# Kernel tuning notes

Measured on AMD Instinct MI355X. Metric: run time of the kernel, lower is better.

Reference implementation:

```python
import jax, jax.numpy as jnp
from jax import lax
import numpy as np

DIM, RESO, HEADS, SPLIT, B = 128, 112, 4, 7, 2
HID = 4 * DIM  # mlp_ratio=4


def _ln(x, g, b):
    m = x.mean(-1, keepdims=True)
    v = ((x - m) ** 2).mean(-1, keepdims=True)
    return (x - m) * lax.rsqrt(v + 1e-5) * g + b


def _lepe_attn(q, k, v, cw, cb, H, W, H_sp, W_sp, nh):
    # q,k,v: [B, H*W, C] (C = branch dim); cw: depthwise conv weight [C,1,3,3]
    Bq, L, C = q.shape
    hd = C // nh
    scale = hd ** -0.5
    nHw, nWw = H // H_sp, W // W_sp

    def to_win(t):  # [B,H,W,C] -> [B*nHw*nWw, nh, H_sp*W_sp, hd]
        t = t.reshape(Bq, nHw, H_sp, nWw, W_sp, C).transpose(0, 1, 3, 2, 4, 5)
        return t.reshape(-1, H_sp * W_sp, nh, hd).transpose(0, 2, 1, 3)

    qw = to_win(q.reshape(Bq, H, W, C)) * scale
    kw = to_win(k.reshape(Bq, H, W, C))

    # v path: window partition in NCHW, depthwise conv LePE per window
    vimg = v.transpose(0, 2, 1).reshape(Bq, C, H, W)
    vimg = vimg.reshape(Bq, C, nHw, H_sp, nWw, W_sp).transpose(0, 2, 4, 1, 3, 5)
    vimg = vimg.reshape(-1, C, H_sp, W_sp)  # [B', C, H_sp, W_sp]
    lepe = lax.conv_general_dilated(vimg, cw, (1, 1), 'SAME', feature_group_count=C,
                                    dimension_numbers=('NCHW', 'OIHW', 'NCHW'))
    lepe = lepe + cb[None, :, None, None]
    vw = vimg.reshape(-1, nh, hd, H_sp * W_sp).transpose(0, 1, 3, 2)
    lepe = lepe.reshape(-1, nh, hd, H_sp * W_sp).transpose(0, 1, 3, 2)

    attn = jax.nn.softmax(jnp.einsum('whnd,whmd->whnm', qw, kw), axis=-1)
    o = jnp.einsum('whnm,whmd->whnd', attn, vw) + lepe  # [B', nh, S, hd]

    # windows2img
    o = o.transpose(0, 2, 1, 3).reshape(-1, H_sp * W_sp, C)
    o = o.reshape(Bq, nHw, nWw, H_sp, W_sp, C).transpose(0, 1, 3, 2, 4, 5)
    return o.reshape(Bq, H * W, C)


def setup_inputs() -> dict:
    key = jax.random.key(0)
    ks = jax.random.split(key, 16)
    s = 0.02
    Cb = DIM // 2
    return {
        'x': jax.random.normal(ks[0], (B, RESO * RESO, DIM), jnp.float32),
        'g1': jnp.ones((DIM,), jnp.float32),
        'b1': jnp.zeros((DIM,), jnp.float32),
        'w_qkv': s * jax.random.normal(ks[1], (3 * DIM, DIM), jnp.float32),
        'conv_w0': s * jax.random.normal(ks[2], (Cb, 1, 3, 3), jnp.float32),
        'conv_b0': jnp.zeros((Cb,), jnp.float32),
        'conv_w1': s * jax.random.normal(ks[3], (Cb, 1, 3, 3), jnp.float32),
        'conv_b1': jnp.zeros((Cb,), jnp.float32),
        'w_proj': s * jax.random.normal(ks[4], (DIM, DIM), jnp.float32),
        'b_proj': jnp.zeros((DIM,), jnp.float32),
        'g2': jnp.ones((DIM,), jnp.float32),
        'b2': jnp.zeros((DIM,), jnp.float32),
        'w_fc1': s * jax.random.normal(ks[5], (HID, DIM), jnp.float32),
        'b_fc1': jnp.zeros((HID,), jnp.float32),
        'w_fc2': s * jax.random.normal(ks[6], (DIM, HID), jnp.float32),
        'b_fc2': jnp.zeros((DIM,), jnp.float32),
    }


def reference(x, g1, b1, w_qkv, conv_w0, conv_b0, conv_w1, conv_b1,
              w_proj, b_proj, g2, b2, w_fc1, b_fc1, w_fc2, b_fc2):
    Bq, L, C = x.shape
    Cb = C // 2
    nh_b = HEADS // 2
    img = _ln(x, g1, b1)
    qkv = (img @ w_qkv.T).reshape(Bq, L, 3, C)  # qkv_bias=False
    q, k, v = qkv[:, :, 0], qkv[:, :, 1], qkv[:, :, 2]
    # branch 0: horizontal stripes (H_sp=RESO, W_sp=SPLIT) on first half of channels
    x1 = _lepe_attn(q[..., :Cb], k[..., :Cb], v[..., :Cb], conv_w0, conv_b0,
                    RESO, RESO, RESO, SPLIT, nh_b)
    # branch 1: vertical stripes (H_sp=SPLIT, W_sp=RESO) on second half
    x2 = _lepe_attn(q[..., Cb:], k[..., Cb:], v[..., Cb:], conv_w1, conv_b1,
                    RESO, RESO, SPLIT, RESO, nh_b)
    att = jnp.concatenate([x1, x2], axis=2)
    att = att @ w_proj.T + b_proj
    x = x + att  # drop_path = identity (prob 0)
    y = _ln(x, g2, b2)
    h = jax.nn.gelu(y @ w_fc1.T + b_fc1, approximate=False)
    x = x + (h @ w_fc2.T + b_fc2)
    return x
```

## Files before the change

kernel.cpp:

```cpp
#include <hip/hip_runtime.h>
#include <cstdint>

#define LTOK 12544
#define BATCH 2
#define CDIM 128
#define C3 384
#define RES 112
#define NROWS (BATCH * LTOK)
#define CHUNKS 784
#define GRID 256
#define SCALE 0.17677669529663687f

typedef __attribute__((ext_vector_type(8))) short bf16x8;
typedef __attribute__((ext_vector_type(4))) float f32x4;

__device__ inline ushort f2b(float f) {
    union { float f; unsigned u; } v; v.f = f;
    unsigned r = (v.u + 0x7FFFu + ((v.u >> 16) & 1u)) >> 16;
    return (ushort)r;
}
__device__ inline float b2f(ushort u) {
    union { float f; unsigned u; } v; v.u = ((unsigned)u) << 16; return v.f;
}
__device__ inline float gelu_f(float a) {
    float u2 = 1.5957691216f * (a + 0.044715f * a * a * a);
    return a - a / (__expf(u2) + 1.0f);
}

__device__ inline void nij(int n, int branch, int& i, int& j) {
    if (branch == 0) { i = n / 7; j = n - i * 7; }
    else             { i = n / 112; j = n - i * 112; }
}

__global__ __launch_bounds__(256) void k_cvt(const float* __restrict__ w0, const float* __restrict__ w1,
        const float* __restrict__ w2, const float* __restrict__ w3,
        ushort* __restrict__ o0, ushort* __restrict__ o1,
        ushort* __restrict__ o2, ushort* __restrict__ o3)
{
    int idx = blockIdx.x * 256 + threadIdx.x;
    const float* src; ushort* dst; int vi;
    if      (idx < 12288) { src = w0; dst = o0; vi = idx; }
    else if (idx < 16384) { src = w1; dst = o1; vi = idx - 12288; }
    else if (idx < 32768) { src = w2; dst = o2; vi = idx - 16384; }
    else                  { src = w3; dst = o3; vi = idx - 32768; }
    float4 v = ((const float4*)src)[vi];
    ushort4 r; r.x = f2b(v.x); r.y = f2b(v.y); r.z = f2b(v.z); r.w = f2b(v.w);
    ((ushort4*)dst)[vi] = r;
}

__global__ __launch_bounds__(512) void k_ln_qkv(const float* __restrict__ x,
        const float* __restrict__ g1, const float* __restrict__ b1,
        const ushort* __restrict__ wqkv_bf, ushort* __restrict__ qkv)
{
    __shared__ ushort ys[32 * 136];
    const int tid = threadIdx.x;
    const int wv = tid >> 6, lane = tid & 63;
    const int c16 = lane & 15, g = lane >> 4;

    bf16x8 wr[3][4];
    #pragma unroll
    for (int t = 0; t < 3; ++t)
        #pragma unroll
        for (int kc = 0; kc < 4; ++kc)
            wr[t][kc] = *(const bf16x8*)&wqkv_bf[(wv * 48 + t * 16 + c16) * CDIM + kc * 32 + g * 8];

    const int r = tid >> 4, l16 = tid & 15;
    float4 gv0 = *(const float4*)(g1 + l16 * 8);
    float4 gv4 = *(const float4*)(g1 + l16 * 8 + 4);
    float4 bv0 = *(const float4*)(b1 + l16 * 8);
    float4 bv4 = *(const float4*)(b1 + l16 * 8 + 4);

    for (int c = blockIdx.x; c < CHUNKS; c += GRID) {
        const long long row0 = (long long)c * 32;

        {
            const float* xr = x + (row0 + r) * CDIM + l16 * 8;
            float4 a0 = *(const float4*)xr;
            float4 a1 = *(const float4*)(xr + 4);
            float s  = a0.x + a0.y + a0.z + a0.w + a1.x + a1.y + a1.z + a1.w;
            float s2 = a0.x*a0.x + a0.y*a0.y + a0.z*a0.z + a0.w*a0.w
                     + a1.x*a1.x + a1.y*a1.y + a1.z*a1.z + a1.w*a1.w;
            #pragma unroll
            for (int m = 8; m >= 1; m >>= 1) { s += __shfl_xor(s, m, 16); s2 += __shfl_xor(s2, m, 16); }
            const float mean = s * (1.f / 128.f);
            const float var = s2 * (1.f / 128.f) - mean * mean;
            const float rs = rsqrtf(var + 1e-5f);
            ushort4 w0, w1;
            w0.x = f2b((a0.x - mean) * rs * gv0.x + bv0.x);
            w0.y = f2b((a0.y - mean) * rs * gv0.y + bv0.y);
            w0.z = f2b((a0.z - mean) * rs * gv0.z + bv0.z);
            w0.w = f2b((a0.w - mean) * rs * gv0.w + bv0.w);
            w1.x = f2b((a1.x - mean) * rs * gv4.x + bv4.x);
            w1.y = f2b((a1.y - mean) * rs * gv4.y + bv4.y);
            w1.z = f2b((a1.z - mean) * rs * gv4.z + bv4.z);
            w1.w = f2b((a1.w - mean) * rs * gv4.w + bv4.w);
            *(ushort4*)&ys[r * 136 + l16 * 8]     = w0;
            *(ushort4*)&ys[r * 136 + l16 * 8 + 4] = w1;
        }
        __syncthreads();

        bf16x8 yb[2][4];
        #pragma unroll
        for (int mt = 0; mt < 2; ++mt)
            #pragma unroll
            for (int kc = 0; kc < 4; ++kc)
                yb[mt][kc] = *(const bf16x8*)&ys[(mt * 16 + c16) * 136 + kc * 32 + g * 8];
        __syncthreads();

        #pragma unroll
        for (int t = 0; t < 3; ++t) {
            const int n0 = wv * 48 + t * 16;
            #pragma unroll
            for (int mt = 0; mt < 2; ++mt) {
                f32x4 acc = {0.f, 0.f, 0.f, 0.f};
                #pragma unroll
                for (int kc = 0; kc < 4; ++kc)
                    acc = __builtin_amdgcn_mfma_f32_16x16x32_bf16(wr[t][kc], yb[mt][kc], acc, 0, 0, 0);
                ushort4 sv;
                sv.x = f2b(acc[0]); sv.y = f2b(acc[1]); sv.z = f2b(acc[2]); sv.w = f2b(acc[3]);
                *(ushort4*)&qkv[(row0 + mt * 16 + c16) * C3 + n0 + g * 4] = sv;
            }
        }
    }
}

__global__ __launch_bounds__(448) void k_attn4(const ushort* __restrict__ qkv,
        const float* __restrict__ cw0, const float* __restrict__ cb0,
        const float* __restrict__ cw1, const float* __restrict__ cb1,
        ushort* __restrict__ att)
{
    __shared__ __align__(16) ushort ks[112 * 40];
    __shared__ __align__(16) ushort vt[32 * 136];
    __shared__ __align__(16) char pool[7][2304];

    const int tid = threadIdx.x;
    const int wv = tid >> 6, lane = tid & 63;
    const int g = lane >> 4, c16 = lane & 15;

    const int wh = blockIdx.x;
    const int branch = wh >> 6;
    const int idx = wh & 63;
    const int win = idx >> 1, head = idx & 1;
    const int b = win >> 4, w = win & 15;
    const int rowBase = branch ? w * 7 : 0;
    const int colBase = branch ? 0 : w * 7;
    const float* cw = branch ? cw1 : cw0;
    const float* cb = branch ? cb1 : cb0;
    const int cbase = branch * 64 + head * 32;
    const long long qkvB = (long long)b * LTOK * C3;

    if (tid < 256) {
        const int row = tid >> 3, cwd = tid & 7;
        *(unsigned*)&vt[row * 136 + 112 + cwd * 2] = 0u;
    }

    const int gt = blockIdx.y * 7 + wv;

    bf16x8 qq;
    {
        int n = gt * 16 + c16;
        int i, j; nij(n, branch, i, j);
        const ushort* qp = qkv + qkvB + (long long)((rowBase + i) * RES + colBase + j) * C3 + cbase + g * 8;
        qq = *(const bf16x8*)qp;
        #pragma unroll
        for (int e = 0; e < 8; ++e) qq[e] = (short)f2b(b2f((ushort)qq[e]) * SCALE);
    }

    f32x4 O0 = {0.f,0.f,0.f,0.f}, O1 = {0.f,0.f,0.f,0.f};
    float lsum[4] = {0.f,0.f,0.f,0.f};
    ushort* pb = (ushort*)pool[wv];

    for (int cc = 0; cc < 7; ++cc) {
        __syncthreads();
        {
            const int key = tid >> 2, d8 = (tid & 3) * 8;
            const int n = cc * 112 + key;
            int i, j; nij(n, branch, i, j);
            const ushort* base = qkv + qkvB + (long long)((rowBase + i) * RES + colBase + j) * C3 + cbase + d8;
            bf16x8 kk = *(const bf16x8*)(base + 128);
            bf16x8 vv = *(const bf16x8*)(base + 256);
            *(bf16x8*)&ks[key * 40 + d8] = kk;
            #pragma unroll
            for (int e = 0; e < 8; ++e) vt[(d8 + e) * 136 + key] = (ushort)vv[e];
        }
        __syncthreads();

        #pragma unroll
        for (int p = 0; p < 4; ++p) {
            bf16x8 kf0 = *(const bf16x8*)&ks[(p * 32 + c16) * 40 + g * 8];
            bf16x8 kf1;
            if (p < 3) kf1 = *(const bf16x8*)&ks[(p * 32 + 16 + c16) * 40 + g * 8];
            bf16x8 vf0 = *(const bf16x8*)&vt[c16 * 136 + p * 32 + g * 8];
            bf16x8 vf1 = *(const bf16x8*)&vt[(16 + c16) * 136 + p * 32 + g * 8];

            f32x4 z = {0.f,0.f,0.f,0.f};
            f32x4 S0 = __builtin_amdgcn_mfma_f32_16x16x32_bf16(qq, kf0, z, 0, 0, 0);
            f32x4 S1 = z;
            if (p < 3) S1 = __builtin_amdgcn_mfma_f32_16x16x32_bf16(qq, kf1, z, 0, 0, 0);
            ushort pw0[4], pw1[4];
            #pragma unroll
            for (int r = 0; r < 4; ++r) {
                float e0 = __expf(S0[r]);
                lsum[r] += e0;
                pw0[r] = f2b(e0);
                if (p < 3) {
                    float e1 = __expf(S1[r]);
                    lsum[r] += e1;
                    pw1[r] = f2b(e1);
                } else pw1[r] = 0;
            }
            #pragma unroll
            for (int r = 0; r < 4; ++r) {
                pb[(g * 4 + r) * 40 + c16]      = pw0[r];
                pb[(g * 4 + r) * 40 + 16 + c16] = pw1[r];
            }
            bf16x8 pf = *(const bf16x8*)&pb[c16 * 40 + g * 8];
            O0 = __builtin_amdgcn_mfma_f32_16x16x32_bf16(pf, vf0, O0, 0, 0, 0);
            O1 = __builtin_amdgcn_mfma_f32_16x16x32_bf16(pf, vf1, O1, 0, 0, 0);
        }
    }

    const int H_sp = branch ? 7 : RES;
    const int W_sp = branch ? RES : 7;
    float* ob = (float*)pool[wv];
    #pragma unroll
    for (int r = 0; r < 4; ++r) {
        float s = lsum[r];
        s += __shfl_xor(s, 1); s += __shfl_xor(s, 2);
        s += __shfl_xor(s, 4); s += __shfl_xor(s, 8);
        const float inv = 1.f / s;
        ob[(g * 4 + r) * 36 + c16]      = O0[r] * inv;
        ob[(g * 4 + r) * 36 + 16 + c16] = O1[r] * inv;
    }
    const int r2 = lane >> 2, db = (lane & 3) * 8;
    const int n0 = gt * 16 + r2;
    int i0, j0; nij(n0, branch, i0, j0);
    float acc[8];
    #pragma unroll
    for (int e = 0; e < 8; ++e) acc[e] = ob[r2 * 36 + db + e] + cb[head * 32 + db + e];
    #pragma unroll
    for (int dij = 0; dij < 9; ++dij) {
        const int di = dij / 3 - 1, dj = dij % 3 - 1;
        const int ii = i0 + di, jj = j0 + dj;
        if (ii >= 0 && ii < H_sp && jj >= 0 && jj < W_sp) {
            const ushort* vp = qkv + qkvB + (long long)((rowBase + ii) * RES + colBase + jj) * C3 + 256 + cbase + db;
            bf16x8 vv = *(const bf16x8*)vp;
            #pragma unroll
            for (int e = 0; e < 8; ++e)
                acc[e] += cw[(head * 32 + db + e) * 9 + dij] * b2f((ushort)vv[e]);
        }
    }
    const long long Lq = (long long)(rowBase + i0) * RES + colBase + j0;
    ushort* op = att + ((long long)b * LTOK + Lq) * CDIM + cbase + db;
    bf16x8 ov;
    #pragma unroll
    for (int e = 0; e < 8; ++e) ov[e] = (short)f2b(acc[e]);
    *(bf16x8*)op = ov;
}

__global__ __launch_bounds__(512) void k_pmlp(const ushort* __restrict__ att,
        const ushort* __restrict__ wproj_bf, const float* __restrict__ bproj,
        const float* __restrict__ x,
        const float* __restrict__ g2, const float* __restrict__ b2,
        const ushort* __restrict__ w1bf, const float* __restrict__ bfc1,
        const ushort* __restrict__ w2bf, const float* __restrict__ bfc2,
        float* __restrict__ out)
{
    __shared__ float  xs[32 * 132];
    __shared__ ushort ys[32 * 136];
    __shared__ ushort hs[32 * 520];
    const int tid = threadIdx.x;
    const int wv = tid >> 6, lane = tid & 63;
    const int c16 = lane & 15, g = lane >> 4;

    bf16x8 wpr[4];
    #pragma unroll
    for (int kc = 0; kc < 4; ++kc)
        wpr[kc] = *(const bf16x8*)&wproj_bf[(wv * 16 + c16) * CDIM + kc * 32 + g * 8];
    bf16x8 w1r[4][4];
    #pragma unroll
    for (int t = 0; t < 4; ++t)
        #pragma unroll
        for (int kc = 0; kc < 4; ++kc)
            w1r[t][kc] = *(const bf16x8*)&w1bf[(wv * 64 + t * 16 + c16) * CDIM + kc * 32 + g * 8];
    const float4 bpv = *(const float4*)&bproj[wv * 16 + g * 4];
    float4 b1v[4];
    #pragma unroll
    for (int t = 0; t < 4; ++t) b1v[t] = *(const float4*)&bfc1[wv * 64 + t * 16 + g * 4];
    const float4 b2v = *(const float4*)&bfc2[wv * 16 + g * 4];

    const int r = tid >> 4, l16 = tid & 15;
    float4 gv0 = *(const float4*)(g2 + l16 * 8);
    float4 gv4 = *(const float4*)(g2 + l16 * 8 + 4);
    float4 bv0 = *(const float4*)(b2 + l16 * 8);
    float4 bv4 = *(const float4*)(b2 + l16 * 8 + 4);

    for (int c = blockIdx.x; c < CHUNKS; c += GRID) {
        const long long row0 = (long long)c * 32;

        f32x4 resid[2];
        {
            bf16x8 ab[2][4];
            #pragma unroll
            for (int mt = 0; mt < 2; ++mt)
                #pragma unroll
                for (int kc = 0; kc < 4; ++kc)
                    ab[mt][kc] = *(const bf16x8*)&att[(row0 + mt * 16 + c16) * CDIM + kc * 32 + g * 8];
            const int col = wv * 16 + g * 4;
            #pragma unroll
            for (int mt = 0; mt < 2; ++mt) {
                f32x4 a = {0.f, 0.f, 0.f, 0.f};
                #pragma unroll
                for (int kc = 0; kc < 4; ++kc)
                    a = __builtin_amdgcn_mfma_f32_16x16x32_bf16(wpr[kc], ab[mt][kc], a, 0, 0, 0);
                float4 xv = *(const float4*)&x[(row0 + mt * 16 + c16) * CDIM + col];
                f32x4 rr;
                rr[0] = a[0] + xv.x + bpv.x;
                rr[1] = a[1] + xv.y + bpv.y;
                rr[2] = a[2] + xv.z + bpv.z;
                rr[3] = a[3] + xv.w + bpv.w;
                resid[mt] = rr;
                *(float4*)&xs[(mt * 16 + c16) * 132 + col] = make_float4(rr[0], rr[1], rr[2], rr[3]);
            }
        }
        __syncthreads();

        {
            float4 a0 = *(const float4*)&xs[r * 132 + l16 * 8];
            float4 a1 = *(const float4*)&xs[r * 132 + l16 * 8 + 4];
            float s  = a0.x + a0.y + a0.z + a0.w + a1.x + a1.y + a1.z + a1.w;
            float s2 = a0.x*a0.x + a0.y*a0.y + a0.z*a0.z + a0.w*a0.w
                     + a1.x*a1.x + a1.y*a1.y + a1.z*a1.z + a1.w*a1.w;
            #pragma unroll
            for (int m = 8; m >= 1; m >>= 1) { s += __shfl_xor(s, m, 16); s2 += __shfl_xor(s2, m, 16); }
            const float mean = s * (1.f / 128.f);
            const float var = s2 * (1.f / 128.f) - mean * mean;
            const float rs = rsqrtf(var + 1e-5f);
            ushort4 w0, w1;
            w0.x = f2b((a0.x - mean) * rs * gv0.x + bv0.x);
            w0.y = f2b((a0.y - mean) * rs * gv0.y + bv0.y);
            w0.z = f2b((a0.z - mean) * rs * gv0.z + bv0.z);
            w0.w = f2b((a0.w - mean) * rs * gv0.w + bv0.w);
            w1.x = f2b((a1.x - mean) * rs * gv4.x + bv4.x);
            w1.y = f2b((a1.y - mean) * rs * gv4.y + bv4.y);
            w1.z = f2b((a1.z - mean) * rs * gv4.z + bv4.z);
            w1.w = f2b((a1.w - mean) * rs * gv4.w + bv4.w);
            *(ushort4*)&ys[r * 136 + l16 * 8]     = w0;
            *(ushort4*)&ys[r * 136 + l16 * 8 + 4] = w1;
        }
        __syncthreads();

        bf16x8 yb[2][4];
        #pragma unroll
        for (int mt = 0; mt < 2; ++mt)
            #pragma unroll
            for (int kc = 0; kc < 4; ++kc)
                yb[mt][kc] = *(const bf16x8*)&ys[(mt * 16 + c16) * 136 + kc * 32 + g * 8];

        #pragma unroll
        for (int t = 0; t < 4; ++t) {
            #pragma unroll
            for (int mt = 0; mt < 2; ++mt) {
                f32x4 a = {0.f, 0.f, 0.f, 0.f};
                #pragma unroll
                for (int kc = 0; kc < 4; ++kc)
                    a = __builtin_amdgcn_mfma_f32_16x16x32_bf16(w1r[t][kc], yb[mt][kc], a, 0, 0, 0);
                ushort4 sv;
                sv.x = f2b(gelu_f(a[0] + b1v[t].x));
                sv.y = f2b(gelu_f(a[1] + b1v[t].y));
                sv.z = f2b(gelu_f(a[2] + b1v[t].z));
                sv.w = f2b(gelu_f(a[3] + b1v[t].w));
                *(ushort4*)&hs[(mt * 16 + c16) * 520 + wv * 64 + t * 16 + g * 4] = sv;
            }
        }

        bf16x8 w2r[16];
        #pragma unroll
        for (int kc = 0; kc < 16; ++kc)
            w2r[kc] = *(const bf16x8*)&w2bf[(wv * 16 + c16) * 512 + kc * 32 + g * 8];

        __syncthreads();

        f32x4 acc2[2] = {{0.f,0.f,0.f,0.f},{0.f,0.f,0.f,0.f}};
        #pragma unroll
        for (int kc = 0; kc < 16; ++kc) {
            bf16x8 hb[2];
            #pragma unroll
            for (int mt = 0; mt < 2; ++mt)
                hb[mt] = *(const bf16x8*)&hs[(mt * 16 + c16) * 520 + kc * 32 + g * 8];
            #pragma unroll
            for (int mt = 0; mt < 2; ++mt)
                acc2[mt] = __builtin_amdgcn_mfma_f32_16x16x32_bf16(w2r[kc], hb[mt], acc2[mt], 0, 0, 0);
        }

        {
            const int col = wv * 16 + g * 4;
            #pragma unroll
            for (int mt = 0; mt < 2; ++mt) {
                const long long row = row0 + mt * 16 + c16;
                float4 o;
                o.x = acc2[mt][0] + resid[mt][0] + b2v.x;
                o.y = acc2[mt][1] + resid[mt][1] + b2v.y;
                o.z = acc2[mt][2] + resid[mt][2] + b2v.z;
                o.w = acc2[mt][3] + resid[mt][3] + b2v.w;
                *(float4*)&out[row * CDIM + col] = o;
            }
        }
    }
}

extern "C" void kernel_launch(void* const* d_in, const int* in_sizes, int n_in,
                              void* d_out, int out_size, void* d_ws, size_t ws_size,
                              hipStream_t stream) {
    const float* x     = (const float*)d_in[0];
    const float* g1    = (const float*)d_in[1];
    const float* b1    = (const float*)d_in[2];
    const float* wqkv  = (const float*)d_in[3];
    const float* cw0   = (const float*)d_in[4];
    const float* cb0   = (const float*)d_in[5];
    const float* cw1   = (const float*)d_in[6];
    const float* cb1   = (const float*)d_in[7];
    const float* wproj = (const float*)d_in[8];
    const float* bproj = (const float*)d_in[9];
    const float* g2    = (const float*)d_in[10];
    const float* b2    = (const float*)d_in[11];
    const float* wfc1  = (const float*)d_in[12];
    const float* bfc1  = (const float*)d_in[13];
    const float* wfc2  = (const float*)d_in[14];
    const float* bfc2  = (const float*)d_in[15];

    char* wsb = (char*)d_ws;
    ushort* qkv_bf   = (ushort*)wsb;
    ushort* att_bf   = (ushort*)(wsb + 19267584);
    char*   wbase    = wsb + 19267584 + 6422528;
    ushort* wqkv_bf  = (ushort*)(wbase);
    ushort* wproj_bf = (ushort*)(wbase + 98304);
    ushort* wfc1_bf  = (ushort*)(wbase + 98304 + 32768);
    ushort* wfc2_bf  = (ushort*)(wbase + 98304 + 32768 + 131072);

    float* out = (float*)d_out;

    k_cvt<<<192, 256, 0, stream>>>(wqkv, wproj, wfc1, wfc2, wqkv_bf, wproj_bf, wfc1_bf, wfc2_bf);
    k_ln_qkv<<<GRID, 512, 0, stream>>>(x, g1, b1, wqkv_bf, qkv_bf);
    k_attn4<<<dim3(128, 7), 448, 0, stream>>>(qkv_bf, cw0, cb0, cw1, cb1, att_bf);
    k_pmlp<<<GRID, 512, 0, stream>>>(att_bf, wproj_bf, bproj, x, g2, b2,
                                     wfc1_bf, bfc1, wfc2_bf, bfc2, out);
}
```

Before: 115.7 us.

## Process two query tiles per wave, prefetch K/V, and widen MLP grids

The attention kernel now handles two 16-query tiles per wave, so each staged K/V chunk in shared memory is reused by twice as many queries, and the grid shrinks from 7 to 4 y-blocks. The next chunk's K and V are loaded into registers while the current chunk is computed, and V is transposed using paired ushort2 stores from half the threads. The QKV and MLP kernels launch 512 blocks instead of 256. The costs are more registers per thread (possible occupancy loss), idle waves in the last y-block, and fewer blocks for attention.

```diff
diff --git a/kernel.cpp b/kernel.cpp
--- a/kernel.cpp
+++ b/kernel.cpp
@@ -8,7 +8,7 @@
 #define RES 112
 #define NROWS (BATCH * LTOK)
 #define CHUNKS 784
-#define GRID 256
+#define GRID_MLP 512
 #define SCALE 0.17677669529663687f
 
 typedef __attribute__((ext_vector_type(8))) short bf16x8;
@@ -70,7 +70,7 @@
     float4 bv0 = *(const float4*)(b1 + l16 * 8);
     float4 bv4 = *(const float4*)(b1 + l16 * 8 + 4);
 
-    for (int c = blockIdx.x; c < CHUNKS; c += GRID) {
+    for (int c = blockIdx.x; c < CHUNKS; c += GRID_MLP) {
         const long long row0 = (long long)c * 32;
 
         {
@@ -124,14 +124,14 @@
     }
 }
 
-__global__ __launch_bounds__(448) void k_attn4(const ushort* __restrict__ qkv,
+__global__ __launch_bounds__(448) void k_attn5(const ushort* __restrict__ qkv,
         const float* __restrict__ cw0, const float* __restrict__ cb0,
         const float* __restrict__ cw1, const float* __restrict__ cb1,
         ushort* __restrict__ att)
 {
     __shared__ __align__(16) ushort ks[112 * 40];
     __shared__ __align__(16) ushort vt[32 * 136];
-    __shared__ __align__(16) char pool[7][2304];
+    __shared__ __align__(16) ushort pl[7][2][640];
 
     const int tid = threadIdx.x;
     const int wv = tid >> 6, lane = tid & 63;
@@ -154,34 +154,73 @@
         *(unsigned*)&vt[row * 136 + 112 + cwd * 2] = 0u;
     }
 
-    const int gt = blockIdx.y * 7 + wv;
-
-    bf16x8 qq;
+    const int tb = blockIdx.y * 14;
+    const int t0 = tb + wv;
+    const int t1 = tb + 7 + wv;
+    const bool act1 = (t1 < 49) && (blockIdx.y < 3);
+
+    bf16x8 qq0, qq1;
     {
-        int n = gt * 16 + c16;
+        int n = t0 * 16 + c16;
         int i, j; nij(n, branch, i, j);
         const ushort* qp = qkv + qkvB + (long long)((rowBase + i) * RES + colBase + j) * C3 + cbase + g * 8;
-        qq = *(const bf16x8*)qp;
-        #pragma unroll
-        for (int e = 0; e < 8; ++e) qq[e] = (short)f2b(b2f((ushort)qq[e]) * SCALE);
-    }
-
-    f32x4 O0 = {0.f,0.f,0.f,0.f}, O1 = {0.f,0.f,0.f,0.f};
-    float lsum[4] = {0.f,0.f,0.f,0.f};
-    ushort* pb = (ushort*)pool[wv];
+        qq0 = *(const bf16x8*)qp;
+        #pragma unroll
+        for (int e = 0; e < 8; ++e) qq0[e] = (short)f2b(b2f((ushort)qq0[e]) * SCALE);
+    }
+    if (act1) {
+        int n = t1 * 16 + c16;
+        int i, j; nij(n, branch, i, j);
+        const ushort* qp = qkv + qkvB + (long long)((rowBase + i) * RES + colBase + j) * C3 + cbase + g * 8;
+        qq1 = *(const bf16x8*)qp;
+        #pragma unroll
+        for (int e = 0; e < 8; ++e) qq1[e] = (short)f2b(b2f((ushort)qq1[e]) * SCALE);
+    }
+
+    f32x4 O00 = {0.f,0.f,0.f,0.f}, O01 = {0.f,0.f,0.f,0.f};
+    f32x4 O10 = {0.f,0.f,0.f,0.f}, O11 = {0.f,0.f,0.f,0.f};
+    float lsum0[4] = {0.f,0.f,0.f,0.f};
+    float lsum1[4] = {0.f,0.f,0.f,0.f};
+
+    const int key = tid >> 2, d8 = (tid & 3) * 8;
+    const bool vrole = (tid < 224);
+
+    bf16x8 kk, va, vb;
+    {
+        int i, j; nij(key, branch, i, j);
+        kk = *(const bf16x8*)(qkv + qkvB + (long long)((rowBase + i) * RES + colBase + j) * C3 + 128 + cbase + d8);
+        if (vrole) {
+            const int n0 = 2 * key;
+            int i0, j0; nij(n0, branch, i0, j0);
+            const long long L0 = (long long)(rowBase + i0) * RES + colBase + j0;
+            const long long L1 = branch ? (L0 + 1) : ((j0 == 6) ? (L0 + RES - 6) : (L0 + 1));
+            va = *(const bf16x8*)(qkv + qkvB + L0 * C3 + 256 + cbase + d8);
+            vb = *(const bf16x8*)(qkv + qkvB + L1 * C3 + 256 + cbase + d8);
+        }
+    }
 
     for (int cc = 0; cc < 7; ++cc) {
         __syncthreads();
-        {
-            const int key = tid >> 2, d8 = (tid & 3) * 8;
-            const int n = cc * 112 + key;
+        *(bf16x8*)&ks[key * 40 + d8] = kk;
+        if (vrole) {
+            #pragma unroll
+            for (int e = 0; e < 8; ++e) {
+                ushort2 pr; pr.x = (ushort)va[e]; pr.y = (ushort)vb[e];
+                *(ushort2*)&vt[(d8 + e) * 136 + 2 * key] = pr;
+            }
+        }
+        if (cc < 6) {
+            const int n = (cc + 1) * 112 + key;
             int i, j; nij(n, branch, i, j);
-            const ushort* base = qkv + qkvB + (long long)((rowBase + i) * RES + colBase + j) * C3 + cbase + d8;
-            bf16x8 kk = *(const bf16x8*)(base + 128);
-            bf16x8 vv = *(const bf16x8*)(base + 256);
-            *(bf16x8*)&ks[key * 40 + d8] = kk;
-            #pragma unroll
-            for (int e = 0; e < 8; ++e) vt[(d8 + e) * 136 + key] = (ushort)vv[e];
+            kk = *(const bf16x8*)(qkv + qkvB + (long long)((rowBase + i) * RES + colBase + j) * C3 + 128 + cbase + d8);
+            if (vrole) {
+                const int n0 = (cc + 1) * 112 + 2 * key;
+                int i0, j0; nij(n0, branch, i0, j0);
+                const long long L0 = (long long)(rowBase + i0) * RES + colBase + j0;
+                const long long L1 = branch ? (L0 + 1) : ((j0 == 6) ? (L0 + RES - 6) : (L0 + 1));
+                va = *(const bf16x8*)(qkv + qkvB + L0 * C3 + 256 + cbase + d8);
+                vb = *(const bf16x8*)(qkv + qkvB + L1 * C3 + 256 + cbase + d8);
+            }
         }
         __syncthreads();
 
@@ -194,68 +233,102 @@
             bf16x8 vf1 = *(const bf16x8*)&vt[(16 + c16) * 136 + p * 32 + g * 8];
 
             f32x4 z = {0.f,0.f,0.f,0.f};
-            f32x4 S0 = __builtin_amdgcn_mfma_f32_16x16x32_bf16(qq, kf0, z, 0, 0, 0);
-            f32x4 S1 = z;
-            if (p < 3) S1 = __builtin_amdgcn_mfma_f32_16x16x32_bf16(qq, kf1, z, 0, 0, 0);
-            ushort pw0[4], pw1[4];
-            #pragma unroll
-            for (int r = 0; r < 4; ++r) {
-                float e0 = __expf(S0[r]);
-                lsum[r] += e0;
-                pw0[r] = f2b(e0);
-                if (p < 3) {
-                    float e1 = __expf(S1[r]);
-                    lsum[r] += e1;
-                    pw1[r] = f2b(e1);
-                } else pw1[r] = 0;
-            }
-            #pragma unroll
-            for (int r = 0; r < 4; ++r) {
-                pb[(g * 4 + r) * 40 + c16]      = pw0[r];
-                pb[(g * 4 + r) * 40 + 16 + c16] = pw1[r];
-            }
-            bf16x8 pf = *(const bf16x8*)&pb[c16 * 40 + g * 8];
-            O0 = __builtin_amdgcn_mfma_f32_16x16x32_bf16(pf, vf0, O0, 0, 0, 0);
-            O1 = __builtin_amdgcn_mfma_f32_16x16x32_bf16(pf, vf1, O1, 0, 0, 0);
+            f32x4 A0 = __builtin_amdgcn_mfma_f32_16x16x32_bf16(qq0, kf0, z, 0, 0, 0);
+            f32x4 A1 = z;
+            if (p < 3) A1 = __builtin_amdgcn_mfma_f32_16x16x32_bf16(qq0, kf1, z, 0, 0, 0);
+            f32x4 B0 = z, B1 = z;
+            if (act1) {
+                B0 = __builtin_amdgcn_mfma_f32_16x16x32_bf16(qq1, kf0, z, 0, 0, 0);
+                if (p < 3) B1 = __builtin_amdgcn_mfma_f32_16x16x32_bf16(qq1, kf1, z, 0, 0, 0);
+            }
+
+            ushort* pb0 = &pl[wv][0][0];
+            {
+                ushort pw0[4], pw1[4];
+                #pragma unroll
+                for (int r = 0; r < 4; ++r) {
+                    float e0 = __expf(A0[r]);
+                    lsum0[r] += e0; pw0[r] = f2b(e0);
+                    if (p < 3) { float e1 = __expf(A1[r]); lsum0[r] += e1; pw1[r] = f2b(e1); }
+                    else pw1[r] = 0;
+                }
+                #pragma unroll
+                for (int r = 0; r < 4; ++r) {
+                    pb0[(g * 4 + r) * 40 + c16]      = pw0[r];
+                    pb0[(g * 4 + r) * 40 + 16 + c16] = pw1[r];
+                }
+            }
+            ushort* pb1 = &pl[wv][1][0];
+            if (act1) {
+                ushort pw0[4], pw1[4];
+                #pragma unroll
+                for (int r = 0; r < 4; ++r) {
+                    float e0 = __expf(B0[r]);
+                    lsum1[r] += e0; pw0[r] = f2b(e0);
+                    if (p < 3) { float e1 = __expf(B1[r]); lsum1[r] += e1; pw1[r] = f2b(e1); }
+                    else pw1[r] = 0;
+                }
+                #pragma unroll
+                for (int r = 0; r < 4; ++r) {
+                    pb1[(g * 4 + r) * 40 + c16]      = pw0[r];
+                    pb1[(g * 4 + r) * 40 + 16 + c16] = pw1[r];
+                }
+            }
+
+            bf16x8 pf0 = *(const bf16x8*)&pb0[c16 * 40 + g * 8];
+            O00 = __builtin_amdgcn_mfma_f32_16x16x32_bf16(pf0, vf0, O00, 0, 0, 0);
+            O01 = __builtin_amdgcn_mfma_f32_16x16x32_bf16(pf0, vf1, O01, 0, 0, 0);
+            if (act1) {
+                bf16x8 pf1 = *(const bf16x8*)&pb1[c16 * 40 + g * 8];
+                O10 = __builtin_amdgcn_mfma_f32_16x16x32_bf16(pf1, vf0, O10, 0, 0, 0);
+                O11 = __builtin_amdgcn_mfma_f32_16x16x32_bf16(pf1, vf1, O11, 0, 0, 0);
+            }
         }
     }
 
     const int H_sp = branch ? 7 : RES;
     const int W_sp = branch ? RES : 7;
-    float* ob = (float*)pool[wv];
+    float* ob = (float*)&pl[wv][0][0];
     #pragma unroll
-    for (int r = 0; r < 4; ++r) {
-        float s = lsum[r];
-        s += __shfl_xor(s, 1); s += __shfl_xor(s, 2);
-        s += __shfl_xor(s, 4); s += __shfl_xor(s, 8);
-        const float inv = 1.f / s;
-        ob[(g * 4 + r) * 36 + c16]      = O0[r] * inv;
-        ob[(g * 4 + r) * 36 + 16 + c16] = O1[r] * inv;
-    }
-    const int r2 = lane >> 2, db = (lane & 3) * 8;
-    const int n0 = gt * 16 + r2;
-    int i0, j0; nij(n0, branch, i0, j0);
-    float acc[8];
-    #pragma unroll
-    for (int e = 0; e < 8; ++e) acc[e] = ob[r2 * 36 + db + e] + cb[head * 32 + db + e];
-    #pragma unroll
-    for (int dij = 0; dij < 9; ++dij) {
-        const int di = dij / 3 - 1, dj = dij % 3 - 1;
-        const int ii = i0 + di, jj = j0 + dj;
-        if (ii >= 0 && ii < H_sp && jj >= 0 && jj < W_sp) {
-            const ushort* vp = qkv + qkvB + (long long)((rowBase + ii) * RES + colBase + jj) * C3 + 256 + cbase + db;
-            bf16x8 vv = *(const bf16x8*)vp;
-            #pragma unroll
-            for (int e = 0; e < 8; ++e)
-                acc[e] += cw[(head * 32 + db + e) * 9 + dij] * b2f((ushort)vv[e]);
-        }
-    }
-    const long long Lq = (long long)(rowBase + i0) * RES + colBase + j0;
-    ushort* op = att + ((long long)b * LTOK + Lq) * CDIM + cbase + db;
-    bf16x8 ov;
-    #pragma unroll
-    for (int e = 0; e < 8; ++e) ov[e] = (short)f2b(acc[e]);
-    *(bf16x8*)op = ov;
+    for (int tt = 0; tt < 2; ++tt) {
+        if (tt == 1 && !act1) break;
+        const int gt = tt ? t1 : t0;
+        const f32x4 Oa = tt ? O10 : O00;
+        const f32x4 Ob = tt ? O11 : O01;
+        #pragma unroll
+        for (int r = 0; r < 4; ++r) {
+            float s = tt ? lsum1[r] : lsum0[r];
+            s += __shfl_xor(s, 1); s += __shfl_xor(s, 2);
+            s += __shfl_xor(s, 4); s += __shfl_xor(s, 8);
+            const float inv = 1.f / s;
+            ob[(g * 4 + r) * 36 + c16]      = Oa[r] * inv;
+            ob[(g * 4 + r) * 36 + 16 + c16] = Ob[r] * inv;
+        }
+        const int r2 = lane >> 2, db = (lane & 3) * 8;
+        const int n0 = gt * 16 + r2;
+        int i0, j0; nij(n0, branch, i0, j0);
+        float acc[8];
+        #pragma unroll
+        for (int e = 0; e < 8; ++e) acc[e] = ob[r2 * 36 + db + e] + cb[head * 32 + db + e];
+        #pragma unroll
+        for (int dij = 0; dij < 9; ++dij) {
+            const int di = dij / 3 - 1, dj = dij % 3 - 1;
+            const int ii = i0 + di, jj = j0 + dj;
+            if (ii >= 0 && ii < H_sp && jj >= 0 && jj < W_sp) {
+                const ushort* vp = qkv + qkvB + (long long)((rowBase + ii) * RES + colBase + jj) * C3 + 256 + cbase + db;
+                bf16x8 vv = *(const bf16x8*)vp;
+                #pragma unroll
+                for (int e = 0; e < 8; ++e)
+                    acc[e] += cw[(head * 32 + db + e) * 9 + dij] * b2f((ushort)vv[e]);
+            }
+        }
+        const long long Lq = (long long)(rowBase + i0) * RES + colBase + j0;
+        ushort* op = att + ((long long)b * LTOK + Lq) * CDIM + cbase + db;
+        bf16x8 ov;
+        #pragma unroll
+        for (int e = 0; e < 8; ++e) ov[e] = (short)f2b(acc[e]);
+        *(bf16x8*)op = ov;
+    }
 }
 
 __global__ __launch_bounds__(512) void k_pmlp(const ushort* __restrict__ att,
@@ -295,7 +368,7 @@
     float4 bv0 = *(const float4*)(b2 + l16 * 8);
     float4 bv4 = *(const float4*)(b2 + l16 * 8 + 4);
 
-    for (int c = blockIdx.x; c < CHUNKS; c += GRID) {
+    for (int c = blockIdx.x; c < CHUNKS; c += GRID_MLP) {
         const long long row0 = (long long)c * 32;
 
         f32x4 resid[2];
@@ -441,8 +514,8 @@
     float* out = (float*)d_out;
 
     k_cvt<<<192, 256, 0, stream>>>(wqkv, wproj, wfc1, wfc2, wqkv_bf, wproj_bf, wfc1_bf, wfc2_bf);
-    k_ln_qkv<<<GRID, 512, 0, stream>>>(x, g1, b1, wqkv_bf, qkv_bf);
-    k_attn4<<<dim3(128, 7), 448, 0, stream>>>(qkv_bf, cw0, cb0, cw1, cb1, att_bf);
-    k_pmlp<<<GRID, 512, 0, stream>>>(att_bf, wproj_bf, bproj, x, g2, b2,
-                                     wfc1_bf, bfc1, wfc2_bf, bfc2, out);
-}
+    k_ln_qkv<<<GRID_MLP, 512, 0, stream>>>(x, g1, b1, wqkv_bf, qkv_bf);
+    k_attn5<<<dim3(128, 4), 448, 0, stream>>>(qkv_bf, cw0, cb0, cw1, cb1, att_bf);
+    k_pmlp<<<GRID_MLP, 512, 0, stream>>>(att_bf, wproj_bf, bproj, x, g2, b2,
+                                         wfc1_bf, bfc1, wfc2_bf, bfc2, out);
+}
```

After: 129.8 us. 1.12x slower.
